# Kernel tuning notes

Measured on AMD Instinct MI355X. Metric: run time of the kernel, lower is better.

## Reference

```python
import jax, jax.numpy as jnp
import numpy as np

H = 512  # hidden_size
L = 2    # num_layers


def setup_inputs() -> dict:
    key = jax.random.key(0)
    ks = jax.random.split(key, 10)
    B, S, I = 64, 512, 512
    s = 1.0 / np.sqrt(H)
    def w(k, shape):
        return jax.random.uniform(k, shape, jnp.float32, -s, s)
    return {
        "x": jax.random.normal(ks[0], (B, S, I), jnp.float32),
        "encoder_h": jax.random.normal(ks[1], (B, 2 * H), jnp.float32),
        "Wih_f": w(ks[2], (L, 3 * H, I)),
        "Whh_f": w(ks[3], (L, 3 * H, H)),
        "bih_f": w(ks[4], (L, 3 * H)),
        "bhh_f": w(ks[5], (L, 3 * H)),
        "Wih_b": w(ks[6], (L, 3 * H, I)),
        "Whh_b": w(ks[7], (L, 3 * H, H)),
        "bih_b": w(ks[8], (L, 3 * H)),
        "bhh_b": w(ks[9], (L, 3 * H)),
    }


def _run_direction(seq, h0, Wih, Whh, bih, bhh):
    """Stacked GRU over time. seq: [B,S,I], h0: [B,H]. Returns ([B,S,H], [B,H]).
    Equivalent to the per-timestep stacked-layer loop in the torch module: each
    layer consumes the previous layer's output stream and its own previous hidden."""
    h_last = h0
    for j in range(L):
        # Precompute input-side gates for the whole sequence (one big GEMM).
        gi = jnp.einsum('bsi,gi->bsg', seq, Wih[j]) + bih[j]  # [B,S,3H]
        Whh_j, bhh_j = Whh[j], bhh[j]

        def step(h, gi_t):
            gh = h @ Whh_j.T + bhh_j                 # [B,3H]
            i_r, i_z, i_n = jnp.split(gi_t, 3, axis=-1)
            h_r, h_z, h_n = jnp.split(gh, 3, axis=-1)
            r = jax.nn.sigmoid(i_r + h_r)
            z = jax.nn.sigmoid(i_z + h_z)
            n = jnp.tanh(i_n + r * h_n)
            h_new = (1.0 - z) * n + z * h
            return h_new, h_new

        h_last, outs = jax.lax.scan(step, h0, jnp.swapaxes(gi, 0, 1))  # outs: [S,B,H]
        seq = jnp.swapaxes(outs, 0, 1)  # [B,S,H] feeds next layer
    return seq, h_last


def reference(x, encoder_h, Wih_f, Whh_f, bih_f, bhh_f, Wih_b, Whh_b, bih_b, bhh_b):
    h0_f = encoder_h[:, :H]
    h0_b = encoder_h[:, H:]
    out_f, h_f = _run_direction(x, h0_f, Wih_f, Whh_f, bih_f, bhh_f)
    x_rev = jnp.flip(x, axis=1)
    out_b_rev, h_b = _run_direction(x_rev, h0_b, Wih_b, Whh_b, bih_b, bhh_b)
    out_b = jnp.flip(out_b_rev, axis=1)
    out = jnp.concatenate([out_f, out_b], axis=2)   # [B,S,2H]
    h = jnp.concatenate([h_f, h_b], axis=1)         # [B,2H]
    return out, h
```

## Files before the change

kernel.cpp:

```cpp
#include <hip/hip_runtime.h>


#define B_ 64
#define S_ 512
#define H_ 512
#define G3_ 1536

typedef __attribute__((ext_vector_type(8))) __bf16 bf16x8;
typedef __attribute__((ext_vector_type(8))) short short8;
typedef __attribute__((ext_vector_type(2))) unsigned long long ull2;
typedef __attribute__((ext_vector_type(4))) float f32x4;
typedef unsigned long long ull;

__device__ __forceinline__ unsigned short f2b(float f) {
  union { float f; unsigned int i; } v; v.f = f;
  unsigned int x = v.i;
  return (unsigned short)((x + 0x7fffu + ((x >> 16) & 1u)) >> 16);
}
__device__ __forceinline__ bf16x8 load8(const unsigned short* p) {
  short8 s = *(const short8*)p;
  return __builtin_bit_cast(bf16x8, s);
}
__device__ __forceinline__ bf16x8 load8f(const float* p) {
  f32x4 a = *(const f32x4*)p, b = *(const f32x4*)(p + 4);
  short8 s;
  s[0] = (short)f2b(a[0]); s[1] = (short)f2b(a[1]);
  s[2] = (short)f2b(a[2]); s[3] = (short)f2b(a[3]);
  s[4] = (short)f2b(b[0]); s[5] = (short)f2b(b[1]);
  s[6] = (short)f2b(b[2]); s[7] = (short)f2b(b[3]);
  return __builtin_bit_cast(bf16x8, s);
}
__device__ __forceinline__ f32x4 mfma16(bf16x8 a, bf16x8 b, f32x4 c) {
  return __builtin_amdgcn_mfma_f32_16x16x32_bf16(a, b, c, 0, 0, 0);
}
__device__ __forceinline__ float sigmoidf_(float x) {
  float e = __expf(-fabsf(x));
  float s = e / (1.0f + e);
  return x >= 0.0f ? 1.0f - s : s;
}
__device__ __forceinline__ float tanhf_(float x) {
  float e = __expf(-2.0f * fabsf(x));
  float r = (1.0f - e) / (1.0f + e);
  return x >= 0.0f ? r : -r;
}
__device__ __forceinline__ bf16x8 load16a(ull* p) {
  ull2 v;
  v[0] = __hip_atomic_load(p, __ATOMIC_RELAXED, __HIP_MEMORY_SCOPE_AGENT);
  v[1] = __hip_atomic_load(p + 1, __ATOMIC_RELAXED, __HIP_MEMORY_SCOPE_AGENT);
  return __builtin_bit_cast(bf16x8, v);
}
__device__ __forceinline__ bf16x8 load16p(const ull* p) {
  ull2 v = *(const ull2*)p;
  return __builtin_bit_cast(bf16x8, v);
}
__device__ __forceinline__ ull pack4(const float* f) {
  ull v = 0;
#pragma unroll
  for (int j = 0; j < 4; ++j) v |= (ull)f2b(f[j]) << (16 * j);
  return v;
}

__global__ void cvt_x(const float* __restrict__ x, ull* __restrict__ xc) {
  int i = blockIdx.x * 256 + threadIdx.x;
  int b = i & 63, cell = (i >> 6) & 63, txx = i >> 12;
  const float* src = x + ((size_t)b * 512 + txx) * 512 + cell * 8;
  float s0[4] = {src[0], src[1], src[2], src[3]};
  float s1[4] = {src[4], src[5], src[6], src[7]};
  size_t o = ((size_t)txx * 4096 + cell * 64 + b) * 2;
  xc[o]     = pack4(s0);
  xc[o + 1] = pack4(s1);
}

__global__ void init_ring(const float* __restrict__ enc, ull* __restrict__ ring) {
  int i = blockIdx.x * 256 + threadIdx.x;
  if (i >= 32768) return;
  int gid = i >> 12;
  int u = i & 4095;
  int d = (gid >> 1) & 1, beta = gid & 1;
  int half = u & 1, b = (u >> 1) & 31, cell = u >> 6;
  const float* e = enc + (size_t)(beta * 32 + b) * 1024 + d * 512 + cell * 8 + half * 4;
  float s[4] = {e[0], e[1], e[2], e[3]};
  ring[(size_t)gid * 32768 + 7 * 4096 + u] = pack4(s);
}

__global__ __launch_bounds__(128) void gru_fused(
    const float* __restrict__ x,
    const ull* __restrict__ xc, int usexc,
    const float* __restrict__ enc,
    const float* __restrict__ WihF, const float* __restrict__ WihB,
    const float* __restrict__ WhhF, const float* __restrict__ WhhB,
    const float* __restrict__ bihF, const float* __restrict__ bihB,
    const float* __restrict__ bhhF, const float* __restrict__ bhhB,
    ull* __restrict__ ring,
    unsigned int* __restrict__ flags,
    float* __restrict__ dout) {
  __shared__ __align__(16) unsigned short wih2[24576];
  __shared__ __align__(16) unsigned short whh2[24576];
  __shared__ float hpub[32 * 20];
  __shared__ int lcnt[8];

  const int tid = threadIdx.x;
  const int lane = tid & 63;
  const int wv = tid >> 6;
  const int wg = (int)blockIdx.x;
  const int l = wg >> 7, d = (wg >> 6) & 1, beta = (wg >> 5) & 1, cb = wg & 31;
  const int gid = ((l * 2 + d) << 1) | beta;
  const int gidA = gid & 3;
  const int gidB = gidA | 4;
  const int colbase = cb * 16;
  const int rowA = lane & 15, kb = lane >> 4;

  const float* Wih = (d ? WihB : WihF) + (size_t)l * G3_ * H_;
  const float* Whh = (d ? WhhB : WhhF) + (size_t)l * G3_ * H_;
  const float* bi = (d ? bihB : bihF) + l * G3_;
  const float* bh = (d ? bhhB : bhhF) + l * G3_;

  if (tid < 8) lcnt[tid] = 0;
  for (int i = tid; i < 3072; i += 128) {
    int gate = i >> 10;
    int rest = i & 1023;
    int kk = rest >> 6;
    int l6 = rest & 63;
    int c = l6 & 15, k = l6 >> 4;
    size_t gro = (size_t)(gate * 512 + colbase + c) * 512 + kk * 32 + k * 8;
    *(short8*)&wih2[i * 8] = __builtin_bit_cast(short8, load8f(Wih + gro));
    *(short8*)&whh2[i * 8] = __builtin_bit_cast(short8, load8f(Whh + gro));
  }
  __syncthreads();

  const int col16 = rowA;
  const int hc = colbase + col16;
  const float brz_r = bi[hc] + bh[hc];
  const float brz_z = bi[512 + hc] + bh[512 + hc];
  const float bi_n = bi[1024 + hc];
  const float bh_n = bh[1024 + hc];

  const int bq = wv * 16 + kb * 4;
  const int arow = wv * 16 + rowA;

  float hm[4];
#pragma unroll
  for (int rg = 0; rg < 4; ++rg)
    hm[rg] = enc[(size_t)(beta * 32 + bq + rg) * 1024 + d * 512 + hc];

  unsigned int* flA = flags + gidA * 1024;
  unsigned int* flB = flags + gidB * 1024;
  unsigned int* flo = flags + gid * 1024;
  ull* ringA = ring + (size_t)gidA * 32768;
  ull* ringl = ring + (size_t)gid * 32768;

  const int pb = tid >> 2;
  const int pq = tid & 3;
  const int pcellL = pq >> 1, phalf = pq & 1;
  const int pc0 = pcellL * 8 + phalf * 4;
  const int pidx = ((2 * cb + pcellL) * 32 + pb) * 2 + phalf;

  for (int t = 0; t < 512; ++t) {
    bf16x8 aIn[16];
    if (l == 0) {
      int txx = d ? (511 - t) : t;
      if (usexc) {
        const ull* xp = xc + (size_t)txx * 8192;
#pragma unroll
        for (int kk = 0; kk < 16; ++kk)
          aIn[kk] = load16p(xp + (size_t)((kk * 4 + kb) * 64 + beta * 32 + arow) * 2);
      } else {
        const float* ap = x + ((size_t)(beta * 32 + arow) * 512 + txx) * 512 + kb * 8;
#pragma unroll
        for (int kk = 0; kk < 16; ++kk) aIn[kk] = load8f(ap + kk * 32);
      }
    }

    {
      const int needA = (l == 0) ? t : (t + 1);
      const int needB = (l == 0) ? (t - 7) : t;
      unsigned int* watch;
      int need;
      if (lane < 32) { watch = flA + lane * 32;        need = needA; }
      else           { watch = flB + (lane - 32) * 32; need = needB; }
      if (need > 0) {
        while (__hip_atomic_load(watch, __ATOMIC_RELAXED,
                                 __HIP_MEMORY_SCOPE_AGENT) < (unsigned)need) {}
      }
    }
    asm volatile("" ::: "memory");

    if (l == 1) {
      ull* rp = ringA + (size_t)(t & 7) * 4096;
#pragma unroll
      for (int kk = 0; kk < 16; ++kk)
        aIn[kk] = load16a(rp + (size_t)((kk * 4 + kb) * 32 + arow) * 2);
    }
    ull* rpo = ringl + (size_t)((t + 7) & 7) * 4096;
    bf16x8 aOwn[16];
#pragma unroll
    for (int kk = 0; kk < 16; ++kk)
      aOwn[kk] = load16a(rpo + (size_t)((kk * 4 + kb) * 32 + arow) * 2);

    f32x4 accr = {0,0,0,0}, accz = {0,0,0,0}, acni = {0,0,0,0}, acnh = {0,0,0,0};
#pragma unroll
    for (int kk = 0; kk < 16; ++kk) {
      const int o = kk * 512 + lane * 8;
      accr = mfma16(aIn[kk],  load8(&wih2[o]), accr);
      accr = mfma16(aOwn[kk], load8(&whh2[o]), accr);
      accz = mfma16(aIn[kk],  load8(&wih2[8192 + o]), accz);
      accz = mfma16(aOwn[kk], load8(&whh2[8192 + o]), accz);
      acni = mfma16(aIn[kk],  load8(&wih2[16384 + o]), acni);
      acnh = mfma16(aOwn[kk], load8(&whh2[16384 + o]), acnh);
    }

#pragma unroll
    for (int rg = 0; rg < 4; ++rg) {
      float r = sigmoidf_(accr[rg] + brz_r);
      float z = sigmoidf_(accz[rg] + brz_z);
      float n = tanhf_(acni[rg] + bi_n + r * (acnh[rg] + bh_n));
      float hnew = (1.0f - z) * n + z * hm[rg];
      hm[rg] = hnew;
      hpub[(bq + rg) * 20 + col16] = hnew;
    }
    asm volatile("" ::: "memory");

    {
      f32x4 v4 = *(f32x4*)&hpub[pb * 20 + pc0];
      float s[4] = {v4[0], v4[1], v4[2], v4[3]};
      __hip_atomic_store(ringl + (size_t)(t & 7) * 4096 + pidx, pack4(s),
                         __ATOMIC_RELAXED, __HIP_MEMORY_SCOPE_AGENT);
    }
    asm volatile("s_waitcnt vmcnt(0)" ::: "memory");

    if (lane == 0) {
      int old = atomicAdd(&lcnt[t & 7], 1);
      if (old == 1) {
        lcnt[t & 7] = 0;
        __hip_atomic_store(flo + cb * 32, (unsigned)(t + 1),
                           __ATOMIC_RELAXED, __HIP_MEMORY_SCOPE_AGENT);
      }
    }

    if (l == 1) {
      const int tox = d ? (511 - t) : t;
#pragma unroll
      for (int rg = 0; rg < 4; ++rg)
        dout[((size_t)(beta * 32 + bq + rg) * 512 + tox) * 1024 + d * 512 + hc] = hm[rg];
    }
  }
}

__global__ void h_epi(float* __restrict__ dout) {
  int i = blockIdx.x * 256 + threadIdx.x;
  if (i >= B_ * 2 * H_) return;
  int b = i >> 10, j = i & 1023;
  int t = (j < H_) ? (S_ - 1) : 0;
  dout[(size_t)B_ * S_ * 2 * H_ + i] = dout[((size_t)b * S_ + t) * (2 * H_) + j];
}

extern "C" void kernel_launch(void* const* d_in, const int* in_sizes, int n_in,
                              void* d_out, int out_size, void* d_ws, size_t ws_size,
                              hipStream_t stream) {
  const float* x    = (const float*)d_in[0];
  const float* enc  = (const float*)d_in[1];
  const float* WihF = (const float*)d_in[2];
  const float* WhhF = (const float*)d_in[3];
  const float* bihF = (const float*)d_in[4];
  const float* bhhF = (const float*)d_in[5];
  const float* WihB = (const float*)d_in[6];
  const float* WhhB = (const float*)d_in[7];
  const float* bihB = (const float*)d_in[8];
  const float* bhhB = (const float*)d_in[9];
  float* out = (float*)d_out;

  char* ws = (char*)d_ws;
  unsigned int* flags = (unsigned int*)ws;
  ull* ring  = (ull*)(ws + 65536);
  ull* xc    = (ull*)(ws + 65536 + 2097152);
  const int usexc = (ws_size >= (size_t)65536 + 2097152 + 33554432) ? 1 : 0;

  (void)hipMemsetAsync(flags, 0, 32768, stream);
  if (usexc) cvt_x<<<8192, 256, 0, stream>>>(x, xc);
  init_ring<<<128, 256, 0, stream>>>(enc, ring);
  gru_fused<<<256, 128, 0, stream>>>(x, xc, usexc, enc,
                                     WihF, WihB, WhhF, WhhB,
                                     bihF, bihB, bhhF, bhhB,
                                     ring, flags, out);
  h_epi<<<256, 256, 0, stream>>>(out);
}
```

Before: 2.319 ms.

## Replace flag-based step sync with tagged ring data polling and deeper overlap

Each published hidden value in the ring now carries a timestep tag in the upper bits of every 32-bit word, so consumers poll the data itself instead of waiting on per-block flags before loading. The ring shrinks to four slots with a new row-major layout. MFMA work is interleaved with polling of successive chunks, and the flag wait that protects against overwriting a slot is moved after the gate math. This is meant to take a flag round-trip off the serial per-timestep critical path, at the cost of doubling ring store traffic and adding unpack and tag-check work.

```diff
diff --git a/kernel.cpp b/kernel.cpp
--- a/kernel.cpp
+++ b/kernel.cpp
@@ -43,44 +43,95 @@
   float r = (1.0f - e) / (1.0f + e);
   return x >= 0.0f ? r : -r;
 }
-__device__ __forceinline__ bf16x8 load16a(ull* p) {
-  ull2 v;
-  v[0] = __hip_atomic_load(p, __ATOMIC_RELAXED, __HIP_MEMORY_SCOPE_AGENT);
-  v[1] = __hip_atomic_load(p + 1, __ATOMIC_RELAXED, __HIP_MEMORY_SCOPE_AGENT);
-  return __builtin_bit_cast(bf16x8, v);
-}
 __device__ __forceinline__ bf16x8 load16p(const ull* p) {
   ull2 v = *(const ull2*)p;
   return __builtin_bit_cast(bf16x8, v);
 }
-__device__ __forceinline__ ull pack4(const float* f) {
-  ull v = 0;
-#pragma unroll
-  for (int j = 0; j < 4; ++j) v |= (ull)f2b(f[j]) << (16 * j);
-  return v;
-}
+
+__device__ __forceinline__ void ld44(ull* p0, ull* p1, ull u[8]) {
+#pragma unroll
+  for (int j = 0; j < 4; ++j) {
+    u[j]     = __hip_atomic_load(p0 + j, __ATOMIC_RELAXED, __HIP_MEMORY_SCOPE_AGENT);
+    u[4 + j] = __hip_atomic_load(p1 + j, __ATOMIC_RELAXED, __HIP_MEMORY_SCOPE_AGENT);
+  }
+}
+__device__ __forceinline__ bool chk8(const ull u[8], unsigned et) {
+  unsigned acc = 0;
+#pragma unroll
+  for (int j = 0; j < 8; ++j) {
+    acc |= (((unsigned)u[j] >> 16) ^ et);
+    acc |= (((unsigned)(u[j] >> 32) >> 16) ^ et);
+  }
+  return acc == 0;
+}
+__device__ __forceinline__ void unp8(const ull u[8], bf16x8* f0, bf16x8* f1) {
+  short8 s0, s1;
+#pragma unroll
+  for (int j = 0; j < 4; ++j) {
+    s0[j * 2]     = (short)((unsigned)u[j] & 0xFFFFu);
+    s0[j * 2 + 1] = (short)((unsigned)(u[j] >> 32) & 0xFFFFu);
+    s1[j * 2]     = (short)((unsigned)u[4 + j] & 0xFFFFu);
+    s1[j * 2 + 1] = (short)((unsigned)(u[4 + j] >> 32) & 0xFFFFu);
+  }
+  *f0 = __builtin_bit_cast(bf16x8, s0);
+  *f1 = __builtin_bit_cast(bf16x8, s1);
+}
+
+#define POLL_ISSUE(BASE, uX, uY)            \
+  ld44((BASE), (BASE) + 16, uX);            \
+  ld44((BASE) + 32, (BASE) + 48, uY);
+
+#define POLL_BODY(BASE, ET, MF, uX, uY)                                       \
+  _Pragma("unroll")                                                           \
+  for (int c = 0; c < 8; ++c) {                                               \
+    ull* uc = (c & 1) ? (uY) : (uX);                                          \
+    if (!chk8(uc, (unsigned)(ET))) {                                          \
+      do {                                                                    \
+        __builtin_amdgcn_s_sleep(1);                                          \
+        ld44((BASE) + c * 32, (BASE) + c * 32 + 16, uc);                      \
+      } while (!chk8(uc, (unsigned)(ET)));                                    \
+    }                                                                         \
+    bf16x8 fA, fB;                                                            \
+    unp8(uc, &fA, &fB);                                                       \
+    if (c < 6) ld44((BASE) + (c + 2) * 32, (BASE) + (c + 2) * 32 + 16, uc);   \
+    MF(c * 2, fA)                                                             \
+    MF(c * 2 + 1, fB)                                                         \
+  }
+
+#define MFMA_IN(kk, f)                                                  \
+  accr = mfma16((f), load8(&wih2[(kk) * 512 + lane * 8]), accr);        \
+  accz = mfma16((f), load8(&wih2[8192 + (kk) * 512 + lane * 8]), accz); \
+  acni = mfma16((f), load8(&wih2[16384 + (kk) * 512 + lane * 8]), acni);
+#define MFMA_OWN(kk, f)                                                 \
+  accr = mfma16((f), load8(&whh2[(kk) * 512 + lane * 8]), accr);        \
+  accz = mfma16((f), load8(&whh2[8192 + (kk) * 512 + lane * 8]), accz); \
+  acnh = mfma16((f), load8(&whh2[16384 + (kk) * 512 + lane * 8]), acnh);
 
 __global__ void cvt_x(const float* __restrict__ x, ull* __restrict__ xc) {
   int i = blockIdx.x * 256 + threadIdx.x;
   int b = i & 63, cell = (i >> 6) & 63, txx = i >> 12;
   const float* src = x + ((size_t)b * 512 + txx) * 512 + cell * 8;
-  float s0[4] = {src[0], src[1], src[2], src[3]};
-  float s1[4] = {src[4], src[5], src[6], src[7]};
+  ull v0 = 0, v1 = 0;
+#pragma unroll
+  for (int j = 0; j < 4; ++j) v0 |= (ull)f2b(src[j]) << (16 * j);
+#pragma unroll
+  for (int j = 0; j < 4; ++j) v1 |= (ull)f2b(src[4 + j]) << (16 * j);
   size_t o = ((size_t)txx * 4096 + cell * 64 + b) * 2;
-  xc[o]     = pack4(s0);
-  xc[o + 1] = pack4(s1);
+  xc[o] = v0;
+  xc[o + 1] = v1;
 }
 
 __global__ void init_ring(const float* __restrict__ enc, ull* __restrict__ ring) {
   int i = blockIdx.x * 256 + threadIdx.x;
-  if (i >= 32768) return;
-  int gid = i >> 12;
-  int u = i & 4095;
+  if (i >= 65536) return;
+  int gid = i >> 13;
+  int u = i & 8191;
   int d = (gid >> 1) & 1, beta = gid & 1;
-  int half = u & 1, b = (u >> 1) & 31, cell = u >> 6;
-  const float* e = enc + (size_t)(beta * 32 + b) * 1024 + d * 512 + cell * 8 + half * 4;
-  float s[4] = {e[0], e[1], e[2], e[3]};
-  ring[(size_t)gid * 32768 + 7 * 4096 + u] = pack4(s);
+  int b = u >> 8;
+  int cp = (u & 255) * 2;
+  const float* e = enc + (size_t)(beta * 32 + b) * 1024 + d * 512 + cp;
+  unsigned w0 = f2b(e[0]), w1 = f2b(e[1]);
+  ring[(size_t)gid * 32768 + 3 * 8192 + u] = (ull)w0 | ((ull)w1 << 32);
 }
 
 __global__ __launch_bounds__(128) void gru_fused(
@@ -96,7 +147,7 @@
     float* __restrict__ dout) {
   __shared__ __align__(16) unsigned short wih2[24576];
   __shared__ __align__(16) unsigned short whh2[24576];
-  __shared__ float hpub[32 * 20];
+  __shared__ float hpub[32 * 24];
   __shared__ int lcnt[8];
 
   const int tid = threadIdx.x;
@@ -106,7 +157,6 @@
   const int l = wg >> 7, d = (wg >> 6) & 1, beta = (wg >> 5) & 1, cb = wg & 31;
   const int gid = ((l * 2 + d) << 1) | beta;
   const int gidA = gid & 3;
-  const int gidB = gidA | 4;
   const int colbase = cb * 16;
   const int rowA = lane & 15, kb = lane >> 4;
 
@@ -143,90 +193,53 @@
   for (int rg = 0; rg < 4; ++rg)
     hm[rg] = enc[(size_t)(beta * 32 + bq + rg) * 1024 + d * 512 + hc];
 
-  unsigned int* flA = flags + gidA * 1024;
-  unsigned int* flB = flags + gidB * 1024;
   unsigned int* flo = flags + gid * 1024;
-  ull* ringA = ring + (size_t)gidA * 32768;
+  ull* ring0 = ring + (size_t)gidA * 32768;
   ull* ringl = ring + (size_t)gid * 32768;
 
   const int pb = tid >> 2;
   const int pq = tid & 3;
-  const int pcellL = pq >> 1, phalf = pq & 1;
-  const int pc0 = pcellL * 8 + phalf * 4;
-  const int pidx = ((2 * cb + pcellL) * 32 + pb) * 2 + phalf;
 
   for (int t = 0; t < 512; ++t) {
-    bf16x8 aIn[16];
+    int need;
+    unsigned int* gw;
+    if (lane < 32) { gw = flo + lane * 32; need = t - 2; }
+    else if (l == 0) { gw = flags + (gid | 4) * 1024 + (lane - 32) * 32; need = t - 3; }
+    else { gw = flo; need = 0; }
+    unsigned gv = (need > 0)
+        ? __hip_atomic_load(gw, __ATOMIC_RELAXED, __HIP_MEMORY_SCOPE_AGENT)
+        : 0xFFFFFFFFu;
+
+    f32x4 accr = {0,0,0,0}, accz = {0,0,0,0}, acni = {0,0,0,0}, acnh = {0,0,0,0};
+    ull* bown = ringl + (size_t)((t + 3) & 3) * 8192 + arow * 256 + kb * 4;
+
     if (l == 0) {
-      int txx = d ? (511 - t) : t;
+      bf16x8 aIn[16];
+      ull uA[8], uB[8];
       if (usexc) {
+        int txx = d ? (511 - t) : t;
         const ull* xp = xc + (size_t)txx * 8192;
 #pragma unroll
         for (int kk = 0; kk < 16; ++kk)
           aIn[kk] = load16p(xp + (size_t)((kk * 4 + kb) * 64 + beta * 32 + arow) * 2);
       } else {
+        int txx = d ? (511 - t) : t;
         const float* ap = x + ((size_t)(beta * 32 + arow) * 512 + txx) * 512 + kb * 8;
 #pragma unroll
         for (int kk = 0; kk < 16; ++kk) aIn[kk] = load8f(ap + kk * 32);
       }
-    }
-
-    {
-      const int needA = (l == 0) ? t : (t + 1);
-      const int needB = (l == 0) ? (t - 7) : t;
-      unsigned int* watch;
-      int need;
-      if (lane < 32) { watch = flA + lane * 32;        need = needA; }
-      else           { watch = flB + (lane - 32) * 32; need = needB; }
-      if (need > 0) {
-        while (__hip_atomic_load(watch, __ATOMIC_RELAXED,
-                                 __HIP_MEMORY_SCOPE_AGENT) < (unsigned)need) {}
-      }
-    }
-    asm volatile("" ::: "memory");
-
-    if (l == 1) {
-      ull* rp = ringA + (size_t)(t & 7) * 4096;
-#pragma unroll
-      for (int kk = 0; kk < 16; ++kk)
-        aIn[kk] = load16a(rp + (size_t)((kk * 4 + kb) * 32 + arow) * 2);
-    }
-    ull* rpo = ringl + (size_t)((t + 7) & 7) * 4096;
-    bf16x8 aOwn[16];
-#pragma unroll
-    for (int kk = 0; kk < 16; ++kk)
-      aOwn[kk] = load16a(rpo + (size_t)((kk * 4 + kb) * 32 + arow) * 2);
-
-    f32x4 accr = {0,0,0,0}, accz = {0,0,0,0}, acni = {0,0,0,0}, acnh = {0,0,0,0};
-#pragma unroll
-    for (int kk = 0; kk < 16; ++kk) {
-      const int o = kk * 512 + lane * 8;
-      accr = mfma16(aIn[kk],  load8(&wih2[o]), accr);
-      accr = mfma16(aOwn[kk], load8(&whh2[o]), accr);
-      accz = mfma16(aIn[kk],  load8(&wih2[8192 + o]), accz);
-      accz = mfma16(aOwn[kk], load8(&whh2[8192 + o]), accz);
-      acni = mfma16(aIn[kk],  load8(&wih2[16384 + o]), acni);
-      acnh = mfma16(aOwn[kk], load8(&whh2[16384 + o]), acnh);
-    }
-
-#pragma unroll
-    for (int rg = 0; rg < 4; ++rg) {
-      float r = sigmoidf_(accr[rg] + brz_r);
-      float z = sigmoidf_(accz[rg] + brz_z);
-      float n = tanhf_(acni[rg] + bi_n + r * (acnh[rg] + bh_n));
-      float hnew = (1.0f - z) * n + z * hm[rg];
-      hm[rg] = hnew;
-      hpub[(bq + rg) * 20 + col16] = hnew;
-    }
-    asm volatile("" ::: "memory");
-
-    {
-      f32x4 v4 = *(f32x4*)&hpub[pb * 20 + pc0];
-      float s[4] = {v4[0], v4[1], v4[2], v4[3]};
-      __hip_atomic_store(ringl + (size_t)(t & 7) * 4096 + pidx, pack4(s),
-                         __ATOMIC_RELAXED, __HIP_MEMORY_SCOPE_AGENT);
-    }
-    asm volatile("s_waitcnt vmcnt(0)" ::: "memory");
+      POLL_ISSUE(bown, uA, uB)
+#pragma unroll
+      for (int kk = 0; kk < 16; ++kk) { MFMA_IN(kk, aIn[kk]) }
+      POLL_BODY(bown, t, MFMA_OWN, uA, uB)
+    } else {
+      ull* bin = ring0 + (size_t)(t & 3) * 8192 + arow * 256 + kb * 4;
+      ull uA[8], uB[8], uC[8], uD[8];
+      POLL_ISSUE(bin, uA, uB)
+      POLL_ISSUE(bown, uC, uD)
+      POLL_BODY(bin, t + 1, MFMA_IN, uA, uB)
+      POLL_BODY(bown, t, MFMA_OWN, uC, uD)
+    }
 
     if (lane == 0) {
       int old = atomicAdd(&lcnt[t & 7], 1);
@@ -235,6 +248,35 @@
         __hip_atomic_store(flo + cb * 32, (unsigned)(t + 1),
                            __ATOMIC_RELAXED, __HIP_MEMORY_SCOPE_AGENT);
       }
+    }
+
+#pragma unroll
+    for (int rg = 0; rg < 4; ++rg) {
+      float r = sigmoidf_(accr[rg] + brz_r);
+      float z = sigmoidf_(accz[rg] + brz_z);
+      float n = tanhf_(acni[rg] + bi_n + r * (acnh[rg] + bh_n));
+      float hnew = (1.0f - z) * n + z * hm[rg];
+      hm[rg] = hnew;
+      hpub[(bq + rg) * 24 + col16] = hnew;
+    }
+    asm volatile("" ::: "memory");
+
+    if (need > 0 && gv < (unsigned)need) {
+      while (__hip_atomic_load(gw, __ATOMIC_RELAXED,
+                               __HIP_MEMORY_SCOPE_AGENT) < (unsigned)need)
+        __builtin_amdgcn_s_sleep(2);
+    }
+
+    {
+      f32x4 v4 = *(f32x4*)&hpub[pb * 24 + pq * 4];
+      unsigned tg = (unsigned)(t + 1) << 16;
+      unsigned w0 = tg | f2b(v4[0]), w1 = tg | f2b(v4[1]);
+      unsigned w2 = tg | f2b(v4[2]), w3 = tg | f2b(v4[3]);
+      ull* pp = ringl + (size_t)(t & 3) * 8192 + pb * 256 + ((colbase + pq * 4) >> 1);
+      __hip_atomic_store(pp, (ull)w0 | ((ull)w1 << 32),
+                         __ATOMIC_RELAXED, __HIP_MEMORY_SCOPE_AGENT);
+      __hip_atomic_store(pp + 1, (ull)w2 | ((ull)w3 << 32),
+                         __ATOMIC_RELAXED, __HIP_MEMORY_SCOPE_AGENT);
     }
 
     if (l == 1) {
@@ -275,9 +317,9 @@
   ull* xc    = (ull*)(ws + 65536 + 2097152);
   const int usexc = (ws_size >= (size_t)65536 + 2097152 + 33554432) ? 1 : 0;
 
-  (void)hipMemsetAsync(flags, 0, 32768, stream);
+  (void)hipMemsetAsync(ws, 0, 65536 + 2097152, stream);
   if (usexc) cvt_x<<<8192, 256, 0, stream>>>(x, xc);
-  init_ring<<<128, 256, 0, stream>>>(enc, ring);
+  init_ring<<<256, 256, 0, stream>>>(enc, ring);
   gru_fused<<<256, 128, 0, stream>>>(x, xc, usexc, enc,
                                      WihF, WihB, WhhF, WhhB,
                                      bihF, bihB, bhhF, bhhB,
```

Result: slower. 4.543 ms (+96.0%).

## Use cache-bypassing vector loads for ring reads and batch layer-1 output stores

Applied to the files above, without the earlier changes.

Replaces the pairs of relaxed atomic 64-bit loads from the inter-block ring with single 128-bit inline-asm global loads carrying sc0 sc1 bits, which skip the non-coherent caches. It issues the own-hidden loads first and adds an explicit waitcnt and sched barrier before the MFMA loop. Layer-1 outputs are staged in shared memory for 8 timesteps and then written as 16-byte vector stores, replacing the per-step scattered scalar stores. This adds LDS use and a hand-written memory-ordering assumption, and the full waitcnt stops loads from overlapping with the MFMA loop.

```diff
diff --git a/kernel.cpp b/kernel.cpp
--- a/kernel.cpp
+++ b/kernel.cpp
@@ -43,32 +43,29 @@
   float r = (1.0f - e) / (1.0f + e);
   return x >= 0.0f ? r : -r;
 }
-__device__ __forceinline__ bf16x8 load16a(ull* p) {
-  ull2 v;
-  v[0] = __hip_atomic_load(p, __ATOMIC_RELAXED, __HIP_MEMORY_SCOPE_AGENT);
-  v[1] = __hip_atomic_load(p + 1, __ATOMIC_RELAXED, __HIP_MEMORY_SCOPE_AGENT);
-  return __builtin_bit_cast(bf16x8, v);
-}
 __device__ __forceinline__ bf16x8 load16p(const ull* p) {
   ull2 v = *(const ull2*)p;
   return __builtin_bit_cast(bf16x8, v);
 }
-__device__ __forceinline__ ull pack4(const float* f) {
-  ull v = 0;
-#pragma unroll
-  for (int j = 0; j < 4; ++j) v |= (ull)f2b(f[j]) << (16 * j);
-  return v;
+__device__ __forceinline__ bf16x8 ld16bypass(const ull* p) {
+  short8 r;
+  asm volatile("global_load_dwordx4 %0, %1, off sc0 sc1"
+               : "=v"(r) : "v"(p) : "memory");
+  return __builtin_bit_cast(bf16x8, r);
 }
 
 __global__ void cvt_x(const float* __restrict__ x, ull* __restrict__ xc) {
   int i = blockIdx.x * 256 + threadIdx.x;
   int b = i & 63, cell = (i >> 6) & 63, txx = i >> 12;
   const float* src = x + ((size_t)b * 512 + txx) * 512 + cell * 8;
-  float s0[4] = {src[0], src[1], src[2], src[3]};
-  float s1[4] = {src[4], src[5], src[6], src[7]};
+  ull v0 = 0, v1 = 0;
+#pragma unroll
+  for (int j = 0; j < 4; ++j) v0 |= (ull)f2b(src[j]) << (16 * j);
+#pragma unroll
+  for (int j = 0; j < 4; ++j) v1 |= (ull)f2b(src[4 + j]) << (16 * j);
   size_t o = ((size_t)txx * 4096 + cell * 64 + b) * 2;
-  xc[o]     = pack4(s0);
-  xc[o + 1] = pack4(s1);
+  xc[o] = v0;
+  xc[o + 1] = v1;
 }
 
 __global__ void init_ring(const float* __restrict__ enc, ull* __restrict__ ring) {
@@ -79,8 +76,10 @@
   int d = (gid >> 1) & 1, beta = gid & 1;
   int half = u & 1, b = (u >> 1) & 31, cell = u >> 6;
   const float* e = enc + (size_t)(beta * 32 + b) * 1024 + d * 512 + cell * 8 + half * 4;
-  float s[4] = {e[0], e[1], e[2], e[3]};
-  ring[(size_t)gid * 32768 + 7 * 4096 + u] = pack4(s);
+  ull v = 0;
+#pragma unroll
+  for (int j = 0; j < 4; ++j) v |= (ull)f2b(e[j]) << (16 * j);
+  ring[(size_t)gid * 32768 + 7 * 4096 + u] = v;
 }
 
 __global__ __launch_bounds__(128) void gru_fused(
@@ -97,6 +96,7 @@
   __shared__ __align__(16) unsigned short wih2[24576];
   __shared__ __align__(16) unsigned short whh2[24576];
   __shared__ float hpub[32 * 20];
+  __shared__ __align__(16) float douts[8][32][20];
   __shared__ int lcnt[8];
 
   const int tid = threadIdx.x;
@@ -152,8 +152,8 @@
   const int pb = tid >> 2;
   const int pq = tid & 3;
   const int pcellL = pq >> 1, phalf = pq & 1;
+  const int pidx = ((2 * cb + pcellL) * 32 + pb) * 2 + phalf;
   const int pc0 = pcellL * 8 + phalf * 4;
-  const int pidx = ((2 * cb + pcellL) * 32 + pb) * 2 + phalf;
 
   for (int t = 0; t < 512; ++t) {
     bf16x8 aIn[16];
@@ -185,17 +185,19 @@
     }
     asm volatile("" ::: "memory");
 
+    bf16x8 aOwn[16];
+    ull* rpo = ringl + (size_t)((t + 7) & 7) * 4096;
+#pragma unroll
+    for (int kk = 0; kk < 16; ++kk)
+      aOwn[kk] = ld16bypass(rpo + (size_t)((kk * 4 + kb) * 32 + arow) * 2);
     if (l == 1) {
       ull* rp = ringA + (size_t)(t & 7) * 4096;
 #pragma unroll
       for (int kk = 0; kk < 16; ++kk)
-        aIn[kk] = load16a(rp + (size_t)((kk * 4 + kb) * 32 + arow) * 2);
-    }
-    ull* rpo = ringl + (size_t)((t + 7) & 7) * 4096;
-    bf16x8 aOwn[16];
-#pragma unroll
-    for (int kk = 0; kk < 16; ++kk)
-      aOwn[kk] = load16a(rpo + (size_t)((kk * 4 + kb) * 32 + arow) * 2);
+        aIn[kk] = ld16bypass(rp + (size_t)((kk * 4 + kb) * 32 + arow) * 2);
+    }
+    asm volatile("s_waitcnt vmcnt(0)" ::: "memory");
+    __builtin_amdgcn_sched_barrier(0);
 
     f32x4 accr = {0,0,0,0}, accz = {0,0,0,0}, acni = {0,0,0,0}, acnh = {0,0,0,0};
 #pragma unroll
@@ -217,13 +219,18 @@
       float hnew = (1.0f - z) * n + z * hm[rg];
       hm[rg] = hnew;
       hpub[(bq + rg) * 20 + col16] = hnew;
+      if (l == 1) douts[t & 7][bq + rg][col16] = hnew;
     }
     asm volatile("" ::: "memory");
 
     {
       f32x4 v4 = *(f32x4*)&hpub[pb * 20 + pc0];
-      float s[4] = {v4[0], v4[1], v4[2], v4[3]};
-      __hip_atomic_store(ringl + (size_t)(t & 7) * 4096 + pidx, pack4(s),
+      ull v = 0;
+      v |= (ull)f2b(v4[0]);
+      v |= (ull)f2b(v4[1]) << 16;
+      v |= (ull)f2b(v4[2]) << 32;
+      v |= (ull)f2b(v4[3]) << 48;
+      __hip_atomic_store(ringl + (size_t)(t & 7) * 4096 + pidx, v,
                          __ATOMIC_RELAXED, __HIP_MEMORY_SCOPE_AGENT);
     }
     asm volatile("s_waitcnt vmcnt(0)" ::: "memory");
@@ -237,11 +244,17 @@
       }
     }
 
-    if (l == 1) {
-      const int tox = d ? (511 - t) : t;
-#pragma unroll
-      for (int rg = 0; rg < 4; ++rg)
-        dout[((size_t)(beta * 32 + bq + rg) * 512 + tox) * 1024 + d * 512 + hc] = hm[rg];
+    if (l == 1 && (t & 7) == 7) {
+      const int fb = tid >> 2;
+      const int fc = (tid & 3) * 4;
+#pragma unroll
+      for (int ts = 0; ts < 8; ++ts) {
+        int tt = t - 7 + ts;
+        int tox = d ? (511 - tt) : tt;
+        f32x4 v = *(f32x4*)&douts[ts][fb][fc];
+        *(f32x4*)&dout[((size_t)(beta * 32 + fb) * 512 + tox) * 1024 +
+                       d * 512 + colbase + fc] = v;
+      }
     }
   }
 }
```

After: 2.442 ms. 1.05x slower.
